# Optimization experiments

Hardware: AMD Instinct MI355X
Metric: run time of the kernel (lower is better)

Reference implementation:

```python
import jax, jax.numpy as jnp
import numpy as np

B_SZ, L, D_MODEL = 2, 1024, 1024
D_INNER, D_STATE, D_CONV = 2048, 16, 4
EPS = 1e-6


def setup_inputs() -> dict:
    key = jax.random.key(0)
    ks = jax.random.split(key, 8)
    def n(k, shape, scale=0.02):
        return jax.random.normal(k, shape, jnp.float32) * scale
    return {
        "x": jax.random.normal(ks[0], (B_SZ, L, D_MODEL), jnp.float32),
        "W_in": n(ks[1], (D_MODEL, 2 * D_INNER)),
        "b_in": jnp.zeros((2 * D_INNER,), jnp.float32),
        "conv_w": n(ks[2], (D_INNER, 1, D_CONV), 0.2),
        "conv_b": jnp.zeros((D_INNER,), jnp.float32),
        "W_xp": n(ks[3], (D_INNER, 2 * D_STATE)),
        "b_xp": jnp.zeros((2 * D_STATE,), jnp.float32),
        "W_dt": n(ks[4], (D_INNER, D_INNER)),
        "b_dt": jnp.full((D_INNER,), -1.0, jnp.float32),
        # torch code does log(randn) (NaN-prone); use log of positive uniform instead
        "A_log": jnp.log(jax.random.uniform(ks[5], (D_INNER, D_STATE), jnp.float32, 0.5, 1.5)),
        "D_skip": jnp.ones((D_INNER,), jnp.float32),
        "W_out": n(ks[6], (D_INNER, D_MODEL)),
        "b_out": jnp.zeros((D_MODEL,), jnp.float32),
        "alpha": jnp.ones((D_MODEL,), jnp.float32),
        "beta": jnp.zeros((D_MODEL,), jnp.float32),
    }


def _selective_scan(xc, delta, A, Bm, Cm, D_skip):
    # xc, delta: (B,L,di); A: (di,ds); Bm, Cm: (B,L,ds)
    dA = jnp.exp(delta[..., None] * A)                     # (B,L,di,ds)
    dBx = (delta * xc)[..., None] * Bm[:, :, None, :]      # (B,L,di,ds)
    h0 = jnp.zeros((xc.shape[0], xc.shape[2], A.shape[1]), xc.dtype)

    def step(h, inp):
        dA_t, dBx_t, C_t = inp
        h = dA_t * h + dBx_t                               # (B,di,ds)
        y_t = jnp.einsum('bds,bs->bd', h, C_t)
        return h, y_t

    _, ys = jax.lax.scan(
        step, h0,
        (dA.transpose(1, 0, 2, 3), dBx.transpose(1, 0, 2, 3), Cm.transpose(1, 0, 2)))
    y = ys.transpose(1, 0, 2)                              # (B,L,di)
    return y + D_skip * xc


def _layernorm(r, alpha, beta):
    # torch LayerNormalization: unbiased std, eps added to std
    mean = jnp.mean(r, axis=-1, keepdims=True)
    diff = r - mean
    var_unb = jnp.sum(diff * diff, axis=-1, keepdims=True) / (r.shape[-1] - 1)
    std = jnp.sqrt(var_unb)
    return alpha * diff / (std + EPS) + beta


def reference(x, W_in, b_in, conv_w, conv_b, W_xp, b_xp, W_dt, b_dt,
              A_log, D_skip, W_out, b_out, alpha, beta):
    residual = x
    xz = x @ W_in + b_in                                   # (B,L,2*di)
    x_in, z = jnp.split(xz, 2, axis=-1)

    # depthwise causal conv1d (torch pads d_conv-1 both sides, slices [:L])
    xt = x_in.transpose(0, 2, 1)                           # (B,di,L)
    xt = jax.lax.conv_general_dilated(
        xt, conv_w, window_strides=(1,), padding=[(D_CONV - 1, 0)],
        feature_group_count=D_INNER, dimension_numbers=('NCH', 'OIH', 'NCH'))
    xt = xt + conv_b[None, :, None]
    x_conv = jax.nn.silu(xt.transpose(0, 2, 1))            # (B,L,di)

    x_proj_out = x_conv @ W_xp + b_xp                      # (B,L,2*ds)
    Bm, Cm = jnp.split(x_proj_out, 2, axis=-1)
    delta = jax.nn.softplus(x_conv @ W_dt + b_dt)          # (B,L,di)
    A = -jnp.exp(A_log)

    y = _selective_scan(x_conv, delta, A, Bm, Cm, D_skip)
    y = y * jax.nn.silu(z)
    out = y @ W_out + b_out                                # (B,L,D)
    return _layernorm(residual + out, alpha, beta)
```

## Files before the change

### kernel.cpp

```cpp
#include <hip/hip_runtime.h>
#include <math.h>

#define B_SZ    2
#define L_SEQ   1024
#define DMODEL  1024
#define DINNER  2048
#define DSTATE  16
#define EPSV    1e-6f

#define CCH 64
#define CS  (L_SEQ / CCH)
#define DT  16
#define SSTR (CCH * DT + 1)

typedef short  bf16x8  __attribute__((ext_vector_type(8)));
typedef float  floatx4 __attribute__((ext_vector_type(4)));
typedef unsigned short ushort8v __attribute__((ext_vector_type(8)));

__device__ __forceinline__ unsigned short f2bf(float f) {
    unsigned int u = __float_as_uint(f);
    unsigned int r = (u + 0x7FFFu + ((u >> 16) & 1u)) >> 16;
    return (unsigned short)r;
}
__device__ __forceinline__ float bf2f(unsigned short u) {
    return __uint_as_float(((unsigned int)u) << 16);
}

__global__ __launch_bounds__(256) void cast_bf16_kernel(
    const float* __restrict__ in, unsigned short* __restrict__ out, int n4)
{
    int i = blockIdx.x * 256 + threadIdx.x;
    if (i >= n4) return;
    float4 v = ((const float4*)in)[i];
    ushort4 o = { f2bf(v.x), f2bf(v.y), f2bf(v.z), f2bf(v.w) };
    ((ushort4*)out)[i] = o;
}

__global__ __launch_bounds__(256) void transpose_cast(
    const float* __restrict__ W, unsigned short* __restrict__ Wt, int K, int N)
{
    __shared__ float tile[32][33];
    const int n0 = blockIdx.x * 32;
    const int k0 = blockIdx.y * 32;
    const int c = threadIdx.x & 31;
    const int r = threadIdx.x >> 5;
#pragma unroll
    for (int i = 0; i < 4; ++i)
        tile[r + 8 * i][c] = W[(size_t)(k0 + r + 8 * i) * N + n0 + c];
    __syncthreads();
#pragma unroll
    for (int i = 0; i < 4; ++i)
        Wt[(size_t)(n0 + r + 8 * i) * K + k0 + c] = f2bf(tile[c][r + 8 * i]);
}

template <int TM, int TN, int MODE>
__global__ __launch_bounds__(256, 3) void gemm_bf16(
    const unsigned short* __restrict__ A, const unsigned short* __restrict__ Bt,
    const float* __restrict__ bias, const float* __restrict__ resid,
    float* __restrict__ C, int M, int N, int K)
{
    constexpr int MI = TM / 32;
    constexpr int NJ = TN / 32;
    constexpr int NLOAD = (TM + TN) / 32;

    __shared__ unsigned short As[TM * 64];
    __shared__ unsigned short Bs[TN * 64];

    const int tid  = threadIdx.x;
    const int wave = tid >> 6;
    const int lane = tid & 63;
    const int m0 = blockIdx.y * TM;
    const int n0 = blockIdx.x * TN;
    const int wm = (wave >> 1) * (TM / 2);
    const int wn = (wave & 1) * (TN / 2);
    const int fr = lane & 15;
    const int kg = lane >> 4;

    int offs[NLOAD];
    unsigned short* lp[NLOAD];
#pragma unroll
    for (int i = 0; i < NLOAD; ++i) {
        const int slot = i * 256 + tid;
        const int row  = slot >> 3;
        const int ch   = slot & 7;
        const int pos  = ch ^ (row & 7);
        if (i < TM / 32) {
            offs[i] = (m0 + row) * K + ch * 8;
            lp[i]   = &As[row * 64 + pos * 8];
        } else {
            const int rb = row - TM;
            offs[i] = (n0 + rb) * K + ch * 8;
            lp[i]   = &Bs[rb * 64 + pos * 8];
        }
    }

    floatx4 acc[MI][NJ] = {};
    bf16x8 pre[NLOAD];

#pragma unroll
    for (int i = 0; i < NLOAD; ++i)
        pre[i] = *(const bf16x8*)((i < TM / 32 ? A : Bt) + offs[i]);
#pragma unroll
    for (int i = 0; i < NLOAD; ++i)
        *(bf16x8*)lp[i] = pre[i];
    __syncthreads();

    for (int kt = 0; kt < K; kt += 64) {
        const bool more = (kt + 64) < K;
        if (more) {
#pragma unroll
            for (int i = 0; i < NLOAD; ++i)
                pre[i] = *(const bf16x8*)((i < TM / 32 ? A : Bt) + offs[i] + kt + 64);
        }

#pragma unroll
        for (int ks = 0; ks < 2; ++ks) {
            const int cq = (ks << 2) | kg;
            bf16x8 af[MI], bfv[NJ];
#pragma unroll
            for (int i = 0; i < MI; ++i) {
                const int row = wm + i * 16 + fr;
                af[i] = *(const bf16x8*)&As[row * 64 + ((cq ^ (row & 7)) << 3)];
            }
#pragma unroll
            for (int j = 0; j < NJ; ++j) {
                const int row = wn + j * 16 + fr;
                bfv[j] = *(const bf16x8*)&Bs[row * 64 + ((cq ^ (row & 7)) << 3)];
            }
#pragma unroll
            for (int i = 0; i < MI; ++i)
#pragma unroll
                for (int j = 0; j < NJ; ++j)
                    acc[i][j] = __builtin_amdgcn_mfma_f32_16x16x32_bf16(
                        af[i], bfv[j], acc[i][j], 0, 0, 0);
        }
        __syncthreads();
        if (more) {
#pragma unroll
            for (int i = 0; i < NLOAD; ++i)
                *(bf16x8*)lp[i] = pre[i];
        }
        __syncthreads();
    }

    const int rq = (lane >> 4) * 4;
#pragma unroll
    for (int i = 0; i < MI; ++i) {
#pragma unroll
        for (int j = 0; j < NJ; ++j) {
            const int col = n0 + wn + j * 16 + fr;
            const float bv = bias[col];
#pragma unroll
            for (int r = 0; r < 4; ++r) {
                const int row = m0 + wm + i * 16 + rq + r;
                float v = acc[i][j][r] + bv;
                if (MODE == 1 || MODE == 3) {
                    v = (v > 20.f) ? v : log1pf(__expf(v));
                } else if (MODE == 2) {
                    v += resid[(size_t)row * N + col];
                }
                if (MODE == 3)
                    ((unsigned short*)C)[(size_t)row * N + col] = f2bf(v);
                else
                    C[(size_t)row * N + col] = v;
            }
        }
    }
}

#define CROWS 4
__global__ __launch_bounds__(256) void conv_xproj(
    const float* __restrict__ xz, const float* __restrict__ conv_w,
    const float* __restrict__ conv_b, const float* __restrict__ W_xp,
    const float* __restrict__ b_xp,
    unsigned short* __restrict__ x_conv_bf, float* __restrict__ BC)
{
    __shared__ float sxc[CROWS][DINNER];
    __shared__ float red[8][CROWS][32];

    const int tid = threadIdx.x;
    const int r0 = blockIdx.x * CROWS;
    const int c8 = tid * 8;

    float wt[8][4];
#pragma unroll
    for (int ci = 0; ci < 8; ++ci) {
        float4 w4 = *(const float4*)&conv_w[(c8 + ci) * 4];
        wt[ci][0] = w4.x; wt[ci][1] = w4.y; wt[ci][2] = w4.z; wt[ci][3] = w4.w;
    }
    float cb[8];
    *(float4*)&cb[0] = *(const float4*)&conv_b[c8];
    *(float4*)&cb[4] = *(const float4*)&conv_b[c8 + 4];

#pragma unroll
    for (int rr = 0; rr < CROWS; ++rr) {
        const int row = r0 + rr;
        const int l = row & (L_SEQ - 1);
        float acc[8];
#pragma unroll
        for (int ci = 0; ci < 8; ++ci) acc[ci] = cb[ci];
#pragma unroll
        for (int h = 0; h < 4; ++h) {
            const int lsrc = l - 3 + h;
            if (lsrc >= 0) {
                float4 a = *(const float4*)&xz[(size_t)(row - 3 + h) * (2 * DINNER) + c8];
                float4 b = *(const float4*)&xz[(size_t)(row - 3 + h) * (2 * DINNER) + c8 + 4];
                acc[0] += a.x * wt[0][h]; acc[1] += a.y * wt[1][h];
                acc[2] += a.z * wt[2][h]; acc[3] += a.w * wt[3][h];
                acc[4] += b.x * wt[4][h]; acc[5] += b.y * wt[5][h];
                acc[6] += b.z * wt[6][h]; acc[7] += b.w * wt[7][h];
            }
        }
        float o[8];
        ushort8v ob;
#pragma unroll
        for (int ci = 0; ci < 8; ++ci) {
            o[ci] = acc[ci] / (1.f + __expf(-acc[ci]));
            sxc[rr][c8 + ci] = o[ci];
            ob[ci] = (short)f2bf(o[ci]);
        }
        *(ushort8v*)&x_conv_bf[(size_t)row * DINNER + c8] = ob;
    }
    __syncthreads();

    const int n = tid & 31;
    const int g = tid >> 5;
    float p[CROWS] = {};
    const int k0 = g * 256;
#pragma unroll 4
    for (int k = k0; k < k0 + 256; ++k) {
        const float wv = W_xp[k * 32 + n];
        p[0] += sxc[0][k] * wv;
        p[1] += sxc[1][k] * wv;
        p[2] += sxc[2][k] * wv;
        p[3] += sxc[3][k] * wv;
    }
#pragma unroll
    for (int rr = 0; rr < CROWS; ++rr) red[g][rr][n] = p[rr];
    __syncthreads();
    if (tid < CROWS * 32) {
        const int rr = tid >> 5;
        const int n2 = tid & 31;
        float s = b_xp[n2];
#pragma unroll
        for (int gg = 0; gg < 8; ++gg) s += red[gg][rr][n2];
        BC[(size_t)(r0 + rr) * 32 + n2] = s;
    }
}

__global__ __launch_bounds__(1024) void scan_kernel(
    const unsigned short* __restrict__ delta_bf,
    const unsigned short* __restrict__ xc_bf,
    const float* __restrict__ BC, const float* __restrict__ A_log,
    const float* __restrict__ D_skip, const float* __restrict__ xz,
    unsigned short* __restrict__ y_bf)
{
    __shared__ float sA[DSTATE * SSTR];
    __shared__ float sH[DSTATE * SSTR];

    const int tid = threadIdx.x;
    const int dl  = tid & (DT - 1);
    const int c   = tid >> 4;
    const int b   = blockIdx.x >> 7;
    const int d0  = (blockIdx.x & 127) * DT;
    const int d   = d0 + dl;

    float Al[DSTATE];
#pragma unroll
    for (int s = 0; s < DSTATE; ++s)
        Al[s] = -__expf(A_log[d * DSTATE + s]) * 1.44269504f;
    const float Dsk = D_skip[d];

    float h[DSTATE];
#pragma unroll
    for (int s = 0; s < DSTATE; ++s) h[s] = 0.f;
    float dsum = 0.f;
    const int l0 = c * CS;
    const size_t row0 = (size_t)(b * L_SEQ + l0);

#pragma unroll 2
    for (int j = 0; j < CS; ++j) {
        const size_t r = row0 + j;
        const float dt = bf2f(delta_bf[r * DINNER + d]);
        const float xc = bf2f(xc_bf[r * DINNER + d]);
        float Bv[DSTATE];
        *(float4*)&Bv[0]  = *(const float4*)&BC[r * 32 + 0];
        *(float4*)&Bv[4]  = *(const float4*)&BC[r * 32 + 4];
        *(float4*)&Bv[8]  = *(const float4*)&BC[r * 32 + 8];
        *(float4*)&Bv[12] = *(const float4*)&BC[r * 32 + 12];
        dsum += dt;
        const float dlx = dt * xc;
#pragma unroll
        for (int s = 0; s < DSTATE; ++s) {
            const float e = exp2f(dt * Al[s]);
            h[s] = e * h[s] + dlx * Bv[s];
        }
    }
#pragma unroll
    for (int s = 0; s < DSTATE; ++s) {
        sH[s * SSTR + c * DT + dl] = h[s];
        sA[s * SSTR + c * DT + dl] = exp2f(Al[s] * dsum);
    }
    __syncthreads();

    if (tid < DSTATE * DT) {
        const int dl2 = tid & (DT - 1);
        const int s2  = tid >> 4;
        float hh = 0.f;
#pragma unroll
        for (int c2 = 0; c2 < CCH; ++c2) {
            const int idx = s2 * SSTR + c2 * DT + dl2;
            const float a  = sA[idx];
            const float he = sH[idx];
            sH[idx] = hh;
            hh = a * hh + he;
        }
    }
    __syncthreads();

#pragma unroll
    for (int s = 0; s < DSTATE; ++s) h[s] = sH[s * SSTR + c * DT + dl];

#pragma unroll 2
    for (int j = 0; j < CS; ++j) {
        const size_t r = row0 + j;
        const float dt = bf2f(delta_bf[r * DINNER + d]);
        const float xc = bf2f(xc_bf[r * DINNER + d]);
        const float z  = xz[r * (2 * DINNER) + DINNER + d];
        float Bv[DSTATE], Cv[DSTATE];
        *(float4*)&Bv[0]  = *(const float4*)&BC[r * 32 + 0];
        *(float4*)&Bv[4]  = *(const float4*)&BC[r * 32 + 4];
        *(float4*)&Bv[8]  = *(const float4*)&BC[r * 32 + 8];
        *(float4*)&Bv[12] = *(const float4*)&BC[r * 32 + 12];
        *(float4*)&Cv[0]  = *(const float4*)&BC[r * 32 + 16];
        *(float4*)&Cv[4]  = *(const float4*)&BC[r * 32 + 20];
        *(float4*)&Cv[8]  = *(const float4*)&BC[r * 32 + 24];
        *(float4*)&Cv[12] = *(const float4*)&BC[r * 32 + 28];
        const float dlx = dt * xc;
        float y = Dsk * xc;
#pragma unroll
        for (int s = 0; s < DSTATE; ++s) {
            const float e = exp2f(dt * Al[s]);
            h[s] = e * h[s] + dlx * Bv[s];
            y += h[s] * Cv[s];
        }
        const float g = z / (1.f + __expf(-z));
        y_bf[r * DINNER + d] = f2bf(y * g);
    }
}

__global__ __launch_bounds__(256) void layernorm_kernel(
    const float* __restrict__ t, const float* __restrict__ alpha,
    const float* __restrict__ beta, float* __restrict__ out)
{
    __shared__ float sred[4];
    __shared__ float sred2[4];
    const int row = blockIdx.x;
    const int tid = threadIdx.x;
    const float* r = t + (size_t)row * DMODEL;

    float4 v = *(const float4*)&r[tid * 4];
    float lsum = v.x + v.y + v.z + v.w;
#pragma unroll
    for (int m = 1; m < 64; m <<= 1) lsum += __shfl_xor(lsum, m);
    if ((tid & 63) == 0) sred[tid >> 6] = lsum;
    __syncthreads();
    const float mean = (sred[0] + sred[1] + sred[2] + sred[3]) * (1.f / DMODEL);

    const float dx = v.x - mean, dy = v.y - mean, dz = v.z - mean, dw = v.w - mean;
    float ls2 = dx * dx + dy * dy + dz * dz + dw * dw;
#pragma unroll
    for (int m = 1; m < 64; m <<= 1) ls2 += __shfl_xor(ls2, m);
    if ((tid & 63) == 0) sred2[tid >> 6] = ls2;
    __syncthreads();
    const float var = (sred2[0] + sred2[1] + sred2[2] + sred2[3]) * (1.f / (DMODEL - 1));
    const float inv = 1.f / (sqrtf(var) + EPSV);

    float4 a4 = *(const float4*)&alpha[tid * 4];
    float4 b4 = *(const float4*)&beta[tid * 4];
    float4 o;
    o.x = a4.x * dx * inv + b4.x;
    o.y = a4.y * dy * inv + b4.y;
    o.z = a4.z * dz * inv + b4.z;
    o.w = a4.w * dw * inv + b4.w;
    *(float4*)&out[(size_t)row * DMODEL + tid * 4] = o;
}

extern "C" void kernel_launch(void* const* d_in, const int* in_sizes, int n_in,
                              void* d_out, int out_size, void* d_ws, size_t ws_size,
                              hipStream_t stream)
{
    const float* x      = (const float*)d_in[0];
    const float* W_in   = (const float*)d_in[1];
    const float* b_in   = (const float*)d_in[2];
    const float* conv_w = (const float*)d_in[3];
    const float* conv_b = (const float*)d_in[4];
    const float* W_xp   = (const float*)d_in[5];
    const float* b_xp   = (const float*)d_in[6];
    const float* W_dt   = (const float*)d_in[7];
    const float* b_dt   = (const float*)d_in[8];
    const float* A_log  = (const float*)d_in[9];
    const float* D_skip = (const float*)d_in[10];
    const float* W_out  = (const float*)d_in[11];
    const float* b_out  = (const float*)d_in[12];
    const float* alpha  = (const float*)d_in[13];
    const float* beta   = (const float*)d_in[14];
    float* out = (float*)d_out;

    const size_t M = (size_t)B_SZ * L_SEQ;
    char* ws = (char*)d_ws;
    float* xz      = (float*)(ws + 0);
    unsigned short* delta_bf = (unsigned short*)(ws + (48u << 20));
    float* BC      = (float*)(ws + (64u << 20));
    unsigned short* x_bf       = (unsigned short*)(ws + (64u << 20) + (512u << 10));
    unsigned short* W_in_t     = (unsigned short*)(ws + (69u << 20));
    unsigned short* W_dt_t     = (unsigned short*)(ws + (77u << 20));
    unsigned short* W_out_t    = (unsigned short*)(ws + (85u << 20));
    unsigned short* x_conv_bf  = (unsigned short*)(ws + (89u << 20));
    unsigned short* ygate_bf   = (unsigned short*)(ws + (77u << 20));
    float* tpre = xz;

    const dim3 blk(256);

    cast_bf16_kernel<<<dim3((unsigned)(M * DMODEL / 4 / 256)), blk, 0, stream>>>(
        x, x_bf, (int)(M * DMODEL / 4));
    transpose_cast<<<dim3(2 * DINNER / 32, DMODEL / 32), blk, 0, stream>>>(
        W_in, W_in_t, DMODEL, 2 * DINNER);
    transpose_cast<<<dim3(DINNER / 32, DINNER / 32), blk, 0, stream>>>(
        W_dt, W_dt_t, DINNER, DINNER);
    transpose_cast<<<dim3(DMODEL / 32, DINNER / 32), blk, 0, stream>>>(
        W_out, W_out_t, DINNER, DMODEL);

    gemm_bf16<128, 64, 0><<<dim3(4096 / 64, 2048 / 128), blk, 0, stream>>>(
        x_bf, W_in_t, b_in, nullptr, xz, 2048, 4096, 1024);

    conv_xproj<<<dim3((unsigned)(M / CROWS)), blk, 0, stream>>>(
        xz, conv_w, conv_b, W_xp, b_xp, x_conv_bf, BC);

    gemm_bf16<128, 64, 3><<<dim3(2048 / 64, 2048 / 128), blk, 0, stream>>>(
        x_conv_bf, W_dt_t, b_dt, nullptr, (float*)delta_bf, 2048, 2048, 2048);

    scan_kernel<<<dim3(B_SZ * (DINNER / DT)), dim3(1024), 0, stream>>>(
        delta_bf, x_conv_bf, BC, A_log, D_skip, xz, ygate_bf);

    gemm_bf16<64, 64, 2><<<dim3(1024 / 64, 2048 / 64), blk, 0, stream>>>(
        ygate_bf, W_out_t, b_out, x, tpre, 2048, 1024, 2048);

    layernorm_kernel<<<dim3((unsigned)M), blk, 0, stream>>>(tpre, alpha, beta, out);
}
```

Before: 299.8 us.

## Store delta transposed from GEMM epilogue and use native exp2 in scan

The delta GEMM epilogue now writes bf16 softplus output transposed (channel-major), so each scan thread loads its 16 delta values with two vector loads and keeps them in registers for both passes. The scan and activation code switch to native exp2/log2 intrinsics for softplus, silu and the state decay, and the scan loops use pointer increments with deeper unroll. The goal is to cut strided global loads and transcendental cost in the scan. The transposed epilogue writes are less coalesced, and the native intrinsics are less accurate.

```diff
diff --git a/kernel.cpp b/kernel.cpp
--- a/kernel.cpp
+++ b/kernel.cpp
@@ -16,6 +16,19 @@
 typedef short  bf16x8  __attribute__((ext_vector_type(8)));
 typedef float  floatx4 __attribute__((ext_vector_type(4)));
 typedef unsigned short ushort8v __attribute__((ext_vector_type(8)));
+
+extern "C" __device__ float __ocml_native_exp2_f32(float);
+extern "C" __device__ float __ocml_native_log2_f32(float);
+
+__device__ __forceinline__ float nexp2(float x) { return __ocml_native_exp2_f32(x); }
+
+__device__ __forceinline__ float softplus_f(float v) {
+    if (v > 20.f) return v;
+    return 0.69314718f * __ocml_native_log2_f32(1.f + nexp2(v * 1.44269504f));
+}
+__device__ __forceinline__ float silu_f(float z) {
+    return z / (1.f + nexp2(z * -1.44269504f));
+}
 
 __device__ __forceinline__ unsigned short f2bf(float f) {
     unsigned int u = __float_as_uint(f);
@@ -144,25 +157,40 @@
     }
 
     const int rq = (lane >> 4) * 4;
-#pragma unroll
-    for (int i = 0; i < MI; ++i) {
-#pragma unroll
-        for (int j = 0; j < NJ; ++j) {
-            const int col = n0 + wn + j * 16 + fr;
-            const float bv = bias[col];
-#pragma unroll
-            for (int r = 0; r < 4; ++r) {
-                const int row = m0 + wm + i * 16 + rq + r;
-                float v = acc[i][j][r] + bv;
-                if (MODE == 1 || MODE == 3) {
-                    v = (v > 20.f) ? v : log1pf(__expf(v));
-                } else if (MODE == 2) {
-                    v += resid[(size_t)row * N + col];
+    if (MODE == 4) {
+        unsigned short* Ct = (unsigned short*)C;
+#pragma unroll
+        for (int i = 0; i < MI; ++i) {
+#pragma unroll
+            for (int j = 0; j < NJ; ++j) {
+                const int col = n0 + wn + j * 16 + fr;
+                const float bv = bias[col];
+                const int row0 = m0 + wm + i * 16 + rq;
+                ushort4 o;
+#pragma unroll
+                for (int r = 0; r < 4; ++r)
+                    (&o.x)[r] = f2bf(softplus_f(acc[i][j][r] + bv));
+                *(ushort4*)&Ct[(size_t)col * M + row0] = o;
+            }
+        }
+    } else {
+#pragma unroll
+        for (int i = 0; i < MI; ++i) {
+#pragma unroll
+            for (int j = 0; j < NJ; ++j) {
+                const int col = n0 + wn + j * 16 + fr;
+                const float bv = bias[col];
+#pragma unroll
+                for (int r = 0; r < 4; ++r) {
+                    const int row = m0 + wm + i * 16 + rq + r;
+                    float v = acc[i][j][r] + bv;
+                    if (MODE == 1) {
+                        v = softplus_f(v);
+                    } else if (MODE == 2) {
+                        v += resid[(size_t)row * N + col];
+                    }
+                    C[(size_t)row * N + col] = v;
                 }
-                if (MODE == 3)
-                    ((unsigned short*)C)[(size_t)row * N + col] = f2bf(v);
-                else
-                    C[(size_t)row * N + col] = v;
             }
         }
     }
@@ -215,7 +243,7 @@
         ushort8v ob;
 #pragma unroll
         for (int ci = 0; ci < 8; ++ci) {
-            o[ci] = acc[ci] / (1.f + __expf(-acc[ci]));
+            o[ci] = silu_f(acc[ci]);
             sxc[rr][c8 + ci] = o[ci];
             ob[ci] = (short)f2bf(o[ci]);
         }
@@ -249,7 +277,7 @@
 }
 
 __global__ __launch_bounds__(1024) void scan_kernel(
-    const unsigned short* __restrict__ delta_bf,
+    const unsigned short* __restrict__ deltaT,
     const unsigned short* __restrict__ xc_bf,
     const float* __restrict__ BC, const float* __restrict__ A_log,
     const float* __restrict__ D_skip, const float* __restrict__ xz,
@@ -271,35 +299,49 @@
         Al[s] = -__expf(A_log[d * DSTATE + s]) * 1.44269504f;
     const float Dsk = D_skip[d];
 
+    const int l0 = c * CS;
+    const int row0 = b * L_SEQ + l0;
+
+    const unsigned short* dpt = deltaT + (size_t)d * (B_SZ * L_SEQ) + row0;
+    bf16x8 dv0 = *(const bf16x8*)dpt;
+    bf16x8 dv1 = *(const bf16x8*)(dpt + 8);
+    float dts[CS];
+    float dsum = 0.f;
+#pragma unroll
+    for (int k = 0; k < 8; ++k) {
+        dts[k]     = bf2f((unsigned short)dv0[k]);
+        dts[8 + k] = bf2f((unsigned short)dv1[k]);
+    }
+#pragma unroll
+    for (int k = 0; k < CS; ++k) dsum += dts[k];
+
     float h[DSTATE];
 #pragma unroll
     for (int s = 0; s < DSTATE; ++s) h[s] = 0.f;
-    float dsum = 0.f;
-    const int l0 = c * CS;
-    const size_t row0 = (size_t)(b * L_SEQ + l0);
-
-#pragma unroll 2
+
+    const unsigned short* xcp = xc_bf + (size_t)row0 * DINNER + d;
+    const float* bcp = BC + (size_t)row0 * 32;
+
+#pragma unroll 4
     for (int j = 0; j < CS; ++j) {
-        const size_t r = row0 + j;
-        const float dt = bf2f(delta_bf[r * DINNER + d]);
-        const float xc = bf2f(xc_bf[r * DINNER + d]);
+        const float dt = dts[j];
+        const float xc = bf2f(xcp[j * DINNER]);
         float Bv[DSTATE];
-        *(float4*)&Bv[0]  = *(const float4*)&BC[r * 32 + 0];
-        *(float4*)&Bv[4]  = *(const float4*)&BC[r * 32 + 4];
-        *(float4*)&Bv[8]  = *(const float4*)&BC[r * 32 + 8];
-        *(float4*)&Bv[12] = *(const float4*)&BC[r * 32 + 12];
-        dsum += dt;
+        *(float4*)&Bv[0]  = *(const float4*)(bcp + j * 32 + 0);
+        *(float4*)&Bv[4]  = *(const float4*)(bcp + j * 32 + 4);
+        *(float4*)&Bv[8]  = *(const float4*)(bcp + j * 32 + 8);
+        *(float4*)&Bv[12] = *(const float4*)(bcp + j * 32 + 12);
         const float dlx = dt * xc;
 #pragma unroll
         for (int s = 0; s < DSTATE; ++s) {
-            const float e = exp2f(dt * Al[s]);
+            const float e = nexp2(dt * Al[s]);
             h[s] = e * h[s] + dlx * Bv[s];
         }
     }
 #pragma unroll
     for (int s = 0; s < DSTATE; ++s) {
         sH[s * SSTR + c * DT + dl] = h[s];
-        sA[s * SSTR + c * DT + dl] = exp2f(Al[s] * dsum);
+        sA[s * SSTR + c * DT + dl] = nexp2(Al[s] * dsum);
     }
     __syncthreads();
 
@@ -321,31 +363,31 @@
 #pragma unroll
     for (int s = 0; s < DSTATE; ++s) h[s] = sH[s * SSTR + c * DT + dl];
 
-#pragma unroll 2
+    const float* zp = xz + (size_t)row0 * (2 * DINNER) + DINNER + d;
+    unsigned short* yp = y_bf + (size_t)row0 * DINNER + d;
+#pragma unroll 4
     for (int j = 0; j < CS; ++j) {
-        const size_t r = row0 + j;
-        const float dt = bf2f(delta_bf[r * DINNER + d]);
-        const float xc = bf2f(xc_bf[r * DINNER + d]);
-        const float z  = xz[r * (2 * DINNER) + DINNER + d];
+        const float dt = dts[j];
+        const float xc = bf2f(xcp[j * DINNER]);
+        const float z  = zp[j * (2 * DINNER)];
         float Bv[DSTATE], Cv[DSTATE];
-        *(float4*)&Bv[0]  = *(const float4*)&BC[r * 32 + 0];
-        *(float4*)&Bv[4]  = *(const float4*)&BC[r * 32 + 4];
-        *(float4*)&Bv[8]  = *(const float4*)&BC[r * 32 + 8];
-        *(float4*)&Bv[12] = *(const float4*)&BC[r * 32 + 12];
-        *(float4*)&Cv[0]  = *(const float4*)&BC[r * 32 + 16];
-        *(float4*)&Cv[4]  = *(const float4*)&BC[r * 32 + 20];
-        *(float4*)&Cv[8]  = *(const float4*)&BC[r * 32 + 24];
-        *(float4*)&Cv[12] = *(const float4*)&BC[r * 32 + 28];
+        *(float4*)&Bv[0]  = *(const float4*)(bcp + j * 32 + 0);
+        *(float4*)&Bv[4]  = *(const float4*)(bcp + j * 32 + 4);
+        *(float4*)&Bv[8]  = *(const float4*)(bcp + j * 32 + 8);
+        *(float4*)&Bv[12] = *(const float4*)(bcp + j * 32 + 12);
+        *(float4*)&Cv[0]  = *(const float4*)(bcp + j * 32 + 16);
+        *(float4*)&Cv[4]  = *(const float4*)(bcp + j * 32 + 20);
+        *(float4*)&Cv[8]  = *(const float4*)(bcp + j * 32 + 24);
+        *(float4*)&Cv[12] = *(const float4*)(bcp + j * 32 + 28);
         const float dlx = dt * xc;
         float y = Dsk * xc;
 #pragma unroll
         for (int s = 0; s < DSTATE; ++s) {
-            const float e = exp2f(dt * Al[s]);
+            const float e = nexp2(dt * Al[s]);
             h[s] = e * h[s] + dlx * Bv[s];
             y += h[s] * Cv[s];
         }
-        const float g = z / (1.f + __expf(-z));
-        y_bf[r * DINNER + d] = f2bf(y * g);
+        yp[j * DINNER] = f2bf(y * silu_f(z));
     }
 }
 
@@ -410,7 +452,7 @@
     const size_t M = (size_t)B_SZ * L_SEQ;
     char* ws = (char*)d_ws;
     float* xz      = (float*)(ws + 0);
-    unsigned short* delta_bf = (unsigned short*)(ws + (48u << 20));
+    unsigned short* deltaT = (unsigned short*)(ws + (48u << 20));
     float* BC      = (float*)(ws + (64u << 20));
     unsigned short* x_bf       = (unsigned short*)(ws + (64u << 20) + (512u << 10));
     unsigned short* W_in_t     = (unsigned short*)(ws + (69u << 20));
@@ -437,11 +479,11 @@
     conv_xproj<<<dim3((unsigned)(M / CROWS)), blk, 0, stream>>>(
         xz, conv_w, conv_b, W_xp, b_xp, x_conv_bf, BC);
 
-    gemm_bf16<128, 64, 3><<<dim3(2048 / 64, 2048 / 128), blk, 0, stream>>>(
-        x_conv_bf, W_dt_t, b_dt, nullptr, (float*)delta_bf, 2048, 2048, 2048);
+    gemm_bf16<128, 64, 4><<<dim3(2048 / 64, 2048 / 128), blk, 0, stream>>>(
+        x_conv_bf, W_dt_t, b_dt, nullptr, (float*)deltaT, 2048, 2048, 2048);
 
     scan_kernel<<<dim3(B_SZ * (DINNER / DT)), dim3(1024), 0, stream>>>(
-        delta_bf, x_conv_bf, BC, A_log, D_skip, xz, ygate_bf);
+        deltaT, x_conv_bf, BC, A_log, D_skip, xz, ygate_bf);
 
     gemm_bf16<64, 64, 2><<<dim3(1024 / 64, 2048 / 64), blk, 0, stream>>>(
         ygate_bf, W_out_t, b_out, x, tpre, 2048, 1024, 2048);
```

Result: faster. 268.9 us (-10.3%).
